# Kernel optimization log

Hardware: AMD Instinct MI355X
Metric: run time of the kernel (lower is better)

The kernel has to match this reference:

```python
import jax, jax.numpy as jnp
import numpy as np

MAX_WINDOW = 256   # maxWindowSize (W)
OUTPUT_DIM = 32    # wavelets per channel (R)


def setup_inputs() -> dict:
    key = jax.random.key(0)
    k1, k2, k3 = jax.random.split(key, 3)
    B, T, C, D = 16, 16384, 8, 1
    W, R = MAX_WINDOW, OUTPUT_DIM
    x = jax.random.normal(k1, (B, T, C, D), dtype=jnp.float32)
    # spatial frequencies in a valid range [3, W/2]
    kValues = 3.0 + jax.random.uniform(k2, (C * R,), dtype=jnp.float32) * (W / 2.0 - 3.0)
    # gaussian widths in [4, W/8] per default minSigmasPerWindow=8
    sigmaValues = 4.0 + jax.random.uniform(k3, (C * R,), dtype=jnp.float32) * (W / 8.0 - 4.0)
    return {"x": x, "kValues": kValues, "sigmaValues": sigmaValues}


def _gabor_bank(kValues, sigmaValues, W, dtype):
    # (C*R, W) real/imag Gabor filters: cos/sin(-2*pi*k*n/W) * gaussian(n; mu=W//2, sigma)
    n = jnp.arange(W, dtype=dtype)
    phase = (-2.0 * np.pi / W) * kValues[:, None] * n[None, :]
    mu = jnp.asarray(W // 2, dtype=dtype)
    inv2s2 = 1.0 / (2.0 * sigmaValues ** 2)                       # (C*R,)
    gauss = (1.0 / jnp.sqrt(2.0 * np.pi * sigmaValues ** 2))[:, None] \
        * jnp.exp(-inv2s2[:, None] * (n - mu) ** 2)               # (C*R, W)
    return jnp.cos(phase) * gauss, jnp.sin(phase) * gauss


def reference(x, kValues, sigmaValues):
    B, T, C, D = x.shape
    W = MAX_WINDOW
    R = kValues.shape[0] // C
    L = T * D
    # (B,T,C,D) -> (B,C,T,D) -> (B,C,L): per-channel 1D signal
    xs = jnp.transpose(x, (0, 2, 1, 3)).reshape(B, C, L)

    fr, fi = _gabor_bank(kValues, sigmaValues, W, x.dtype)        # (C*R, W) each
    dn = ('NCH', 'OIH', 'NCH')
    pad = [(W - 1, W - 1)]  # 'full' correlation -> L + W - 1 outputs

    def dconv(f):
        # grouped (depthwise) conv: output channel c*R+j correlates x[:,c] with f[c*R+j]
        return jax.lax.conv_general_dilated(
            xs, f[:, None, :], window_strides=(1,), padding=pad,
            dimension_numbers=dn, feature_group_count=C)

    cr = dconv(fr)                                                # (B, C*R, L+W-1)
    ci = dconv(fi)
    power = cr ** 2 + ci ** 2
    # theano slice [W/2-1 : -W/2] -> length L
    power = power[:, :, W // 2 - 1: (L + W - 1) - W // 2]         # (B, C*R, L)
    # theano's full-mode row conv against a 1-row input flips the filter-row axis
    p = power.reshape(B, C, R, L)[:, :, ::-1, :]                  # (B, C, R, L)
    out = jnp.transpose(p, (0, 3, 1, 2)).reshape(B, L, C * R)     # (B, L, C*R)
    return out
```

## Files before the change

### kernel.cpp

```cpp
#include <hip/hip_runtime.h>
#include <hip/hip_bf16.h>

#define B_ 16
#define T_ 16384
#define C_ 8
#define L_ 16384
#define W_ 256
#define R_ 32

typedef __bf16 bf16x8 __attribute__((ext_vector_type(8)));
typedef float f32x4 __attribute__((ext_vector_type(4)));

__global__ void xconv_kernel(const float* __restrict__ x,
                             unsigned short* __restrict__ xt) {
  unsigned idx = blockIdx.x * 256u + threadIdx.x;
  unsigned t = idx & (L_ - 1);
  unsigned c = (idx >> 14) & (C_ - 1);
  unsigned b = idx >> 17;
  float v = x[((size_t)b * T_ + t) * C_ + c];
  __bf16 h = (__bf16)v;
  xt[idx] = __builtin_bit_cast(unsigned short, h);
}

__global__ void gen_filters_kernel(const float* __restrict__ kv,
                                   const float* __restrict__ sv,
                                   unsigned short* __restrict__ Fg) {
  unsigned idx = blockIdx.x * 256u + threadIdx.x;
  unsigned w = idx & (W_ - 1);
  unsigned j = (idx >> 8) & 63u;
  unsigned c = idx >> 14;
  unsigned r = j & 31u;
  unsigned pidx = c * 32u + (31u - r);
  float k  = kv[pidx];
  float sg = sv[pidx];
  float phase = (-6.283185307179586f / (float)W_) * k * (float)w;
  float dn = (float)w - (float)(W_ / 2);
  float var2 = 2.0f * sg * sg;
  float g = (1.0f / sqrtf(3.14159265358979f * var2)) * expf(-(dn * dn) / var2);
  float s, cth;
  sincosf(phase, &s, &cth);
  float v = (j < 32u) ? cth * g : s * g;
  __bf16 h = (__bf16)v;
  Fg[idx] = __builtin_bit_cast(unsigned short, h);
}

__global__ __launch_bounds__(256, 2) void wavelet_main_kernel(
    const unsigned short* __restrict__ xt,
    const unsigned short* __restrict__ Fg,
    float* __restrict__ out)
{
  __shared__ __align__(16) unsigned int Fs[64 * 132];
  __shared__ unsigned int xe[256];
  __shared__ unsigned int xo[256];

  const int tid = threadIdx.x;
  const unsigned bid = blockIdx.x;
  const int tb = bid & 63;
  const int c  = (bid >> 6) & 7;
  const int b  = bid >> 9;
  const int t0 = tb << 8;

  {
    const uint4* Fg4 = reinterpret_cast<const uint4*>(Fg + (size_t)c * (64 * 256));
    #pragma unroll
    for (int it = 0; it < 8; ++it) {
      int i = it * 256 + tid;
      uint4 v = Fg4[i];
      int j  = i >> 5;
      int wq = (i & 31) << 2;
      *reinterpret_cast<uint4*>(&Fs[j * 132 + wq]) = v;
    }
  }

  {
    const unsigned short* xrow = xt + ((size_t)b * C_ + c) * L_;
    int i0 = 2 * tid;
    int ta = t0 - 128 + i0;
    unsigned int v0 = (ta     >= 0 && ta     < L_) ? (unsigned int)xrow[ta]     : 0u;
    unsigned int v1 = (ta + 1 >= 0 && ta + 1 < L_) ? (unsigned int)xrow[ta + 1] : 0u;
    unsigned int v2 = (ta + 2 >= 0 && ta + 2 < L_) ? (unsigned int)xrow[ta + 2] : 0u;
    xe[tid] = v0 | (v1 << 16);
    xo[tid] = v1 | (v2 << 16);
  }
  __syncthreads();

  const int lane = tid & 63;
  const int wv   = tid >> 6;
  const int quad = lane >> 4;
  const int lrow = lane & 15;

  f32x4 acc[4][4];
  #pragma unroll
  for (int mt = 0; mt < 4; ++mt)
    #pragma unroll
    for (int nt = 0; nt < 4; ++nt)
      acc[mt][nt] = (f32x4){0.f, 0.f, 0.f, 0.f};

  #pragma unroll
  for (int kk = 0; kk < 8; ++kk) {
    const int k0 = kk * 32;

    bf16x8 bfr[4];
    #pragma unroll
    for (int nt = 0; nt < 4; ++nt) {
      const uint4 v = *reinterpret_cast<const uint4*>(
          &Fs[(nt * 16 + lrow) * 132 + (k0 >> 1) + quad * 4]);
      bfr[nt] = __builtin_bit_cast(bf16x8, v);
    }

    bf16x8 afr[4];
    #pragma unroll
    for (int mt = 0; mt < 4; ++mt) {
      const int s = wv * 64 + mt * 16 + lrow + k0 + quad * 8;
      const unsigned int* src = (s & 1) ? xo : xe;
      const int d0 = s >> 1;
      uint4 v;
      v.x = src[d0]; v.y = src[d0 + 1]; v.z = src[d0 + 2]; v.w = src[d0 + 3];
      afr[mt] = __builtin_bit_cast(bf16x8, v);
    }

    #pragma unroll
    for (int mt = 0; mt < 4; ++mt)
      #pragma unroll
      for (int nt = 0; nt < 4; ++nt)
        acc[mt][nt] = __builtin_amdgcn_mfma_f32_16x16x32_bf16(
            afr[mt], bfr[nt], acc[mt][nt], 0, 0, 0);
  }

  const size_t obase = ((size_t)b * L_) * 256 + (size_t)c * 32 + lrow;
  #pragma unroll
  for (int mt = 0; mt < 4; ++mt) {
    #pragma unroll
    for (int i = 0; i < 4; ++i) {
      const int t = t0 + wv * 64 + mt * 16 + quad * 4 + i;
      float* orow = out + obase + (size_t)t * 256;
      orow[0]  = acc[mt][0][i] * acc[mt][0][i] + acc[mt][2][i] * acc[mt][2][i];
      orow[16] = acc[mt][1][i] * acc[mt][1][i] + acc[mt][3][i] * acc[mt][3][i];
    }
  }
}

extern "C" void kernel_launch(void* const* d_in, const int* in_sizes, int n_in,
                              void* d_out, int out_size, void* d_ws, size_t ws_size,
                              hipStream_t stream) {
  const float* x  = (const float*)d_in[0];
  const float* kv = (const float*)d_in[1];
  const float* sv = (const float*)d_in[2];
  float* out = (float*)d_out;

  unsigned short* xt = (unsigned short*)d_ws;
  unsigned short* Fg = xt + (size_t)B_ * C_ * L_;

  hipLaunchKernelGGL(xconv_kernel, dim3((B_ * C_ * L_) / 256), dim3(256), 0, stream,
                     x, xt);
  hipLaunchKernelGGL(gen_filters_kernel, dim3((C_ * 64 * W_) / 256), dim3(256), 0, stream,
                     kv, sv, Fg);
  hipLaunchKernelGGL(wavelet_main_kernel, dim3(B_ * C_ * (L_ / 256)), dim3(256), 0, stream,
                     xt, Fg, out);
}
```

Baseline: 282.6 us.

## Make wavelet blocks persistent over 16 time tiles with double-buffered input windows

The main kernel now launches 512 blocks, each covering 4096 time steps for one (batch, channel). The filter bank is loaded into shared memory once per block instead of once per 256-step tile, and the next input window is prefetched into registers while the current tile's MFMAs run. Input windows are stored pre-expanded as aligned 8-element rows so A fragments come from a single 16-byte LDS read. The transpose/convert kernel now uses vectorized float4 loads, an LDS transpose, and uint4 stores. The trade-off is fewer blocks, 512 versus the earlier 8192, which lowers occupancy slack and parallelism on a GPU with many CUs.

```diff
diff --git a/kernel.cpp b/kernel.cpp
--- a/kernel.cpp
+++ b/kernel.cpp
@@ -13,13 +13,33 @@
 
 __global__ void xconv_kernel(const float* __restrict__ x,
                              unsigned short* __restrict__ xt) {
-  unsigned idx = blockIdx.x * 256u + threadIdx.x;
-  unsigned t = idx & (L_ - 1);
-  unsigned c = (idx >> 14) & (C_ - 1);
-  unsigned b = idx >> 17;
-  float v = x[((size_t)b * T_ + t) * C_ + c];
-  __bf16 h = (__bf16)v;
-  xt[idx] = __builtin_bit_cast(unsigned short, h);
+  __shared__ unsigned short Xl[8][264];
+  const int tid = threadIdx.x;
+  const int b = blockIdx.x >> 6;
+  const int t0 = (blockIdx.x & 63) << 8;
+  const float4* src = reinterpret_cast<const float4*>(x + ((size_t)b * T_ + t0) * C_);
+  #pragma unroll
+  for (int h = 0; h < 2; ++h) {
+    const int vi = h * 256 + tid;
+    float4 v = src[vi];
+    const int e = vi * 4;
+    const int tt = e >> 3;
+    const int c0 = e & 7;
+    Xl[c0 + 0][tt] = __builtin_bit_cast(unsigned short, (__bf16)v.x);
+    Xl[c0 + 1][tt] = __builtin_bit_cast(unsigned short, (__bf16)v.y);
+    Xl[c0 + 2][tt] = __builtin_bit_cast(unsigned short, (__bf16)v.z);
+    Xl[c0 + 3][tt] = __builtin_bit_cast(unsigned short, (__bf16)v.w);
+  }
+  __syncthreads();
+  const int c = tid >> 5;
+  const int toff = (tid & 31) * 8;
+  const unsigned short* p = &Xl[c][toff];
+  uint4 o;
+  o.x = (unsigned)p[0] | ((unsigned)p[1] << 16);
+  o.y = (unsigned)p[2] | ((unsigned)p[3] << 16);
+  o.z = (unsigned)p[4] | ((unsigned)p[5] << 16);
+  o.w = (unsigned)p[6] | ((unsigned)p[7] << 16);
+  *reinterpret_cast<uint4*>(xt + ((size_t)b * C_ + c) * L_ + t0 + toff) = o;
 }
 
 __global__ void gen_filters_kernel(const float* __restrict__ kv,
@@ -40,8 +60,7 @@
   float s, cth;
   sincosf(phase, &s, &cth);
   float v = (j < 32u) ? cth * g : s * g;
-  __bf16 h = (__bf16)v;
-  Fg[idx] = __builtin_bit_cast(unsigned short, h);
+  Fg[idx] = __builtin_bit_cast(unsigned short, (__bf16)v);
 }
 
 __global__ __launch_bounds__(256, 2) void wavelet_main_kernel(
@@ -50,93 +69,132 @@
     float* __restrict__ out)
 {
   __shared__ __align__(16) unsigned int Fs[64 * 132];
-  __shared__ unsigned int xe[256];
-  __shared__ unsigned int xo[256];
+  __shared__ __align__(16) unsigned int Xs[2][2048];
 
   const int tid = threadIdx.x;
   const unsigned bid = blockIdx.x;
-  const int tb = bid & 63;
-  const int c  = (bid >> 6) & 7;
-  const int b  = bid >> 9;
-  const int t0 = tb << 8;
+  const int p = bid & 3;
+  const int c = (bid >> 2) & 7;
+  const int b = bid >> 5;
+  const unsigned short* __restrict__ xrow = xt + ((size_t)b * C_ + c) * L_;
 
   {
     const uint4* Fg4 = reinterpret_cast<const uint4*>(Fg + (size_t)c * (64 * 256));
     #pragma unroll
-    for (int it = 0; it < 8; ++it) {
-      int i = it * 256 + tid;
+    for (int i8 = 0; i8 < 8; ++i8) {
+      int i = i8 * 256 + tid;
       uint4 v = Fg4[i];
-      int j  = i >> 5;
-      int wq = (i & 31) << 2;
-      *reinterpret_cast<uint4*>(&Fs[j * 132 + wq]) = v;
+      *reinterpret_cast<uint4*>(&Fs[(i >> 5) * 132 + ((i & 31) << 2)]) = v;
     }
   }
 
-  {
-    const unsigned short* xrow = xt + ((size_t)b * C_ + c) * L_;
-    int i0 = 2 * tid;
-    int ta = t0 - 128 + i0;
-    unsigned int v0 = (ta     >= 0 && ta     < L_) ? (unsigned int)xrow[ta]     : 0u;
-    unsigned int v1 = (ta + 1 >= 0 && ta + 1 < L_) ? (unsigned int)xrow[ta + 1] : 0u;
-    unsigned int v2 = (ta + 2 >= 0 && ta + 2 < L_) ? (unsigned int)xrow[ta + 2] : 0u;
-    xe[tid] = v0 | (v1 << 16);
-    xo[tid] = v1 | (v2 << 16);
-  }
-  __syncthreads();
+  const int s0 = 2 * tid;
+
+  auto load_window = [&](int t0, uint4& v0, uint4& v1) {
+    const int gbase = t0 - 128 + (s0 & ~7);
+    if (t0 >= 128 && t0 + 392 <= L_) {
+      const uint4* g = reinterpret_cast<const uint4*>(xrow + gbase);
+      v0 = g[0];
+      v1 = g[1];
+    } else {
+      unsigned int d[8];
+      #pragma unroll
+      for (int q = 0; q < 8; ++q) {
+        int g0 = gbase + 2 * q, g1 = g0 + 1;
+        unsigned lo = (g0 >= 0 && g0 < L_) ? (unsigned)xrow[g0] : 0u;
+        unsigned hi = (g1 >= 0 && g1 < L_) ? (unsigned)xrow[g1] : 0u;
+        d[q] = lo | (hi << 16);
+      }
+      v0 = make_uint4(d[0], d[1], d[2], d[3]);
+      v1 = make_uint4(d[4], d[5], d[6], d[7]);
+    }
+  };
+
+  auto write_window = [&](int buf, const uint4& v0, const uint4& v1) {
+    const bool a2 = (tid & 2) != 0;
+    unsigned u0 = a2 ? v0.z : v0.x;
+    unsigned u1 = a2 ? v0.w : v0.y;
+    unsigned u2 = a2 ? v1.x : v0.z;
+    unsigned u3 = a2 ? v1.y : v0.w;
+    unsigned u4 = a2 ? v1.z : v1.x;
+    unsigned u5 = a2 ? v1.w : v1.y;
+    const bool a1 = (tid & 1) != 0;
+    unsigned e0 = a1 ? u1 : u0;
+    unsigned e1 = a1 ? u2 : u1;
+    unsigned e2 = a1 ? u3 : u2;
+    unsigned e3 = a1 ? u4 : u3;
+    unsigned e4 = a1 ? u5 : u4;
+    uint4 c0 = make_uint4(e0, e1, e2, e3);
+    uint4 c1 = make_uint4((e0 >> 16) | (e1 << 16),
+                          (e1 >> 16) | (e2 << 16),
+                          (e2 >> 16) | (e3 << 16),
+                          (e3 >> 16) | (e4 << 16));
+    *reinterpret_cast<uint4*>(&Xs[buf][s0 * 4]) = c0;
+    *reinterpret_cast<uint4*>(&Xs[buf][s0 * 4 + 4]) = c1;
+  };
 
   const int lane = tid & 63;
   const int wv   = tid >> 6;
   const int quad = lane >> 4;
   const int lrow = lane & 15;
-
-  f32x4 acc[4][4];
-  #pragma unroll
-  for (int mt = 0; mt < 4; ++mt)
-    #pragma unroll
-    for (int nt = 0; nt < 4; ++nt)
-      acc[mt][nt] = (f32x4){0.f, 0.f, 0.f, 0.f};
-
-  #pragma unroll
-  for (int kk = 0; kk < 8; ++kk) {
-    const int k0 = kk * 32;
-
-    bf16x8 bfr[4];
-    #pragma unroll
-    for (int nt = 0; nt < 4; ++nt) {
-      const uint4 v = *reinterpret_cast<const uint4*>(
-          &Fs[(nt * 16 + lrow) * 132 + (k0 >> 1) + quad * 4]);
-      bfr[nt] = __builtin_bit_cast(bf16x8, v);
+  const size_t obase = ((size_t)b * L_) * 256 + (size_t)c * 32 + lrow;
+
+  auto compute = [&](int buf, int t0) {
+    f32x4 acc[4][4];
+    #pragma unroll
+    for (int mt = 0; mt < 4; ++mt)
+      #pragma unroll
+      for (int nt = 0; nt < 4; ++nt)
+        acc[mt][nt] = (f32x4){0.f, 0.f, 0.f, 0.f};
+
+    #pragma unroll
+    for (int kk = 0; kk < 8; ++kk) {
+      bf16x8 bfr[4], afr[4];
+      #pragma unroll
+      for (int nt = 0; nt < 4; ++nt)
+        bfr[nt] = __builtin_bit_cast(bf16x8, *reinterpret_cast<const uint4*>(
+            &Fs[(nt * 16 + lrow) * 132 + kk * 16 + quad * 4]));
+      #pragma unroll
+      for (int mt = 0; mt < 4; ++mt) {
+        const int s = wv * 64 + mt * 16 + lrow + kk * 32 + quad * 8;
+        afr[mt] = __builtin_bit_cast(bf16x8, *reinterpret_cast<const uint4*>(
+            &Xs[buf][s * 4]));
+      }
+      #pragma unroll
+      for (int mt = 0; mt < 4; ++mt)
+        #pragma unroll
+        for (int nt = 0; nt < 4; ++nt)
+          acc[mt][nt] = __builtin_amdgcn_mfma_f32_16x16x32_bf16(
+              afr[mt], bfr[nt], acc[mt][nt], 0, 0, 0);
     }
 
-    bf16x8 afr[4];
-    #pragma unroll
-    for (int mt = 0; mt < 4; ++mt) {
-      const int s = wv * 64 + mt * 16 + lrow + k0 + quad * 8;
-      const unsigned int* src = (s & 1) ? xo : xe;
-      const int d0 = s >> 1;
-      uint4 v;
-      v.x = src[d0]; v.y = src[d0 + 1]; v.z = src[d0 + 2]; v.w = src[d0 + 3];
-      afr[mt] = __builtin_bit_cast(bf16x8, v);
-    }
-
     #pragma unroll
     for (int mt = 0; mt < 4; ++mt)
       #pragma unroll
-      for (int nt = 0; nt < 4; ++nt)
-        acc[mt][nt] = __builtin_amdgcn_mfma_f32_16x16x32_bf16(
-            afr[mt], bfr[nt], acc[mt][nt], 0, 0, 0);
-  }
-
-  const size_t obase = ((size_t)b * L_) * 256 + (size_t)c * 32 + lrow;
-  #pragma unroll
-  for (int mt = 0; mt < 4; ++mt) {
-    #pragma unroll
-    for (int i = 0; i < 4; ++i) {
-      const int t = t0 + wv * 64 + mt * 16 + quad * 4 + i;
-      float* orow = out + obase + (size_t)t * 256;
-      orow[0]  = acc[mt][0][i] * acc[mt][0][i] + acc[mt][2][i] * acc[mt][2][i];
-      orow[16] = acc[mt][1][i] * acc[mt][1][i] + acc[mt][3][i] * acc[mt][3][i];
-    }
+      for (int i = 0; i < 4; ++i) {
+        const int t = t0 + wv * 64 + mt * 16 + quad * 4 + i;
+        float* orow = out + obase + (size_t)t * 256;
+        orow[0]  = acc[mt][0][i] * acc[mt][0][i] + acc[mt][2][i] * acc[mt][2][i];
+        orow[16] = acc[mt][1][i] * acc[mt][1][i] + acc[mt][3][i] * acc[mt][3][i];
+      }
+  };
+
+  const int tstart = p * 4096;
+  {
+    uint4 v0, v1;
+    load_window(tstart, v0, v1);
+    write_window(0, v0, v1);
+  }
+  __syncthreads();
+
+  #pragma unroll 1
+  for (int it = 0; it < 16; ++it) {
+    const int t0 = tstart + it * 256;
+    uint4 v0, v1;
+    if (it < 15) load_window(t0 + 256, v0, v1);
+    compute(it & 1, t0);
+    if (it < 15) write_window((it + 1) & 1, v0, v1);
+    __syncthreads();
   }
 }
 
@@ -151,10 +209,10 @@
   unsigned short* xt = (unsigned short*)d_ws;
   unsigned short* Fg = xt + (size_t)B_ * C_ * L_;
 
-  hipLaunchKernelGGL(xconv_kernel, dim3((B_ * C_ * L_) / 256), dim3(256), 0, stream,
+  hipLaunchKernelGGL(xconv_kernel, dim3(B_ * (L_ / 256)), dim3(256), 0, stream,
                      x, xt);
   hipLaunchKernelGGL(gen_filters_kernel, dim3((C_ * 64 * W_) / 256), dim3(256), 0, stream,
                      kv, sv, Fg);
-  hipLaunchKernelGGL(wavelet_main_kernel, dim3(B_ * C_ * (L_ / 256)), dim3(256), 0, stream,
+  hipLaunchKernelGGL(wavelet_main_kernel, dim3(512), dim3(256), 0, stream,
                      xt, Fg, out);
 }
```

Measured after the change: 290.0 us. 2.6% more time.
